# Kernel optimization log

Hardware: AMD Instinct MI355X
Metric: run time of the kernel (lower is better)

## Reference

```python
import jax, jax.numpy as jnp
import numpy as np
import math

PS = 8          # patch_size
OUT_C = 16      # out_channels
D_MODEL = 64
P_STATE = 32
BANDLIMIT = 1.0
STEP_SCALE = 1.0  # dt1 reference rate


def _ln(x, g, b, eps=1e-5):
    mu = jnp.mean(x, -1, keepdims=True)
    var = jnp.mean((x - mu) ** 2, -1, keepdims=True)
    return (x - mu) * jax.lax.rsqrt(var + eps) * g + b


def _forward(x, W_embed, b_embed, g1, beta1, Lambda_re, Lambda_im, B_re, B_im,
             C_re, C_im, D, log_step, g2, beta2, W_enc, W_dec, g3, beta3, W_out, b_out):
    b, t, h, w = x.shape
    hp, wp = h // PS, w // PS
    n = hp * wp
    # patchify: [b,t,h,w] -> [b,t,n,ps*ps]
    xp = x.reshape(b, t, hp, PS, wp, PS).transpose(0, 1, 2, 4, 3, 5).reshape(b, t, n, PS * PS)
    xe = xp @ W_embed.T + b_embed                              # [b,t,n,d]
    u = xe.transpose(0, 2, 1, 3).reshape(b * n, t, D_MODEL)    # [(b n), t, d]

    # ---- S5Block: pre-norm -> diagonal SSM -> gelu + residual -> GEGLU FFN ----
    fx = _ln(u, g1, beta1)
    Lam = Lambda_re + 1j * Lambda_im                           # [P] complex eigenvalues
    step = STEP_SCALE * jnp.exp(log_step)                      # [P]
    Lbar = jnp.exp(Lam * step)                                 # ZOH: A_bar
    Bbar = ((Lbar - 1.0) / Lam)[:, None] * (B_re + 1j * B_im)  # ZOH: B_bar [P,d]
    # bandlimit mask on C (freqs = step*|Im(Lambda)|/(2pi) < bandlimit/2)
    freqs = step * jnp.abs(Lambda_im) / (2.0 * math.pi)
    mask = (freqs < BANDLIMIT * 0.5).astype(C_re.dtype)
    Cc = (C_re + 1j * C_im) * mask[None, :]                    # [d,P]

    Bu = jnp.einsum('ntd,pd->ntp', fx.astype(jnp.complex64), Bbar)   # [(bn),t,P]
    A = jnp.broadcast_to(Lbar.astype(jnp.complex64), (1, t, P_STATE))

    def comb(e1, e2):
        a1, b1 = e1
        a2, b2 = e2
        return a1 * a2, a2 * b1 + b2

    _, xs = jax.lax.associative_scan(comb, (A, Bu), axis=1)    # x_k = A*x_{k-1} + Bu_k (x_0 = 0)
    ys = jnp.einsum('ntp,dp->ntd', xs, Cc).real + fx * D       # y = Re(C x) + D u
    xb = jax.nn.gelu(ys, approximate=False) + fx

    fx2 = _ln(xb, g2, beta2)
    enc = fx2 @ W_enc.T                                        # [(bn),t,2d]
    a, gate = jnp.split(enc, 2, axis=-1)
    xb = (a * jax.nn.gelu(gate, approximate=False)) @ W_dec.T + fx2

    # ---- take last timestep, project, unpatchify ----
    x_last = xb[:, -1, :]                                      # [(bn), d]
    proj = _ln(x_last, g3, beta3) @ W_out.T + b_out            # [(bn), C*ps*ps]
    y = proj.reshape(b, hp, wp, OUT_C, PS, PS).transpose(0, 3, 1, 4, 2, 5).reshape(b, OUT_C, h, w)
    return y


def setup_inputs() -> dict:
    key = jax.random.key(0)
    ks = jax.random.split(key, 12)
    d, P, pp = D_MODEL, P_STATE, PS * PS
    return dict(
        x=jax.random.normal(ks[0], (8, 15, 480, 640), jnp.float32),
        W_embed=jax.random.normal(ks[1], (d, pp), jnp.float32) / math.sqrt(pp),
        b_embed=jnp.zeros((d,), jnp.float32),
        g1=jnp.ones((d,), jnp.float32), beta1=jnp.zeros((d,), jnp.float32),
        Lambda_re=-0.5 * jnp.ones((P,), jnp.float32),
        Lambda_im=math.pi * (1.0 + jnp.arange(P, dtype=jnp.float32)),
        B_re=jax.random.normal(ks[2], (P, d), jnp.float32) / math.sqrt(d),
        B_im=jax.random.normal(ks[3], (P, d), jnp.float32) / math.sqrt(d),
        C_re=jax.random.normal(ks[4], (d, P), jnp.float32) / math.sqrt(P),
        C_im=jax.random.normal(ks[5], (d, P), jnp.float32) / math.sqrt(P),
        D=jax.random.normal(ks[6], (d,), jnp.float32),
        log_step=jax.random.uniform(ks[7], (P,), jnp.float32, math.log(1e-3), math.log(1e-1)),
        g2=jnp.ones((d,), jnp.float32), beta2=jnp.zeros((d,), jnp.float32),
        W_enc=jax.random.normal(ks[8], (2 * d, d), jnp.float32) / math.sqrt(d),
        W_dec=jax.random.normal(ks[9], (d, d), jnp.float32) / math.sqrt(d),
        g3=jnp.ones((d,), jnp.float32), beta3=jnp.zeros((d,), jnp.float32),
        W_out=jax.random.normal(ks[10], (OUT_C * pp, d), jnp.float32) / math.sqrt(d),
        b_out=jnp.zeros((OUT_C * pp,), jnp.float32),
    )


def reference(x, W_embed, b_embed, g1, beta1, Lambda_re, Lambda_im, B_re, B_im,
              C_re, C_im, D, log_step, g2, beta2, W_enc, W_dec, g3, beta3, W_out, b_out):
    return _forward(x, W_embed, b_embed, g1, beta1, Lambda_re, Lambda_im, B_re, B_im,
                    C_re, C_im, D, log_step, g2, beta2, W_enc, W_dec, g3, beta3, W_out, b_out)
```

## Files before the change

### kernel.cpp

```cpp
#include <hip/hip_runtime.h>
#include <math.h>


typedef __attribute__((ext_vector_type(8))) short short8;
typedef __attribute__((ext_vector_type(4))) float f32x4;

#define MFMA16(a, b, c) __builtin_amdgcn_mfma_f32_16x16x32_bf16((a), (b), (c), 0, 0, 0)

__device__ __forceinline__ short f2bf(float f) {
  union { float f; unsigned u; } v; v.f = f;
  unsigned r = (v.u + 0x7fffu + ((v.u >> 16) & 1u)) >> 16;
  return (short)r;
}
__device__ __forceinline__ float geluf(float x) {
  return 0.5f * x * (1.0f + erff(x * 0.70710678118654752f));
}
__device__ __forceinline__ short8 packfrag(const f32x4& a, const f32x4& b) {
  short8 o;
  o[0] = f2bf(a[0]); o[1] = f2bf(a[1]); o[2] = f2bf(a[2]); o[3] = f2bf(a[3]);
  o[4] = f2bf(b[0]); o[5] = f2bf(b[1]); o[6] = f2bf(b[2]); o[7] = f2bf(b[3]);
  return o;
}
__device__ __forceinline__ int ecmap(int i, int m) {
  return (i >> 1) * 32 + (m >> 2) * 8 + (i & 1) * 4 + (m & 3);
}
__device__ __forceinline__ int swz(int b) {
  return b ^ (((b >> 2) ^ (b >> 6)) & 0x60) ^ (((b >> 3) ^ (b >> 9)) & 0x10);
}
__device__ __forceinline__ void bbar_factors(const float* Lre, const float* Lim,
                                             const float* lstep, int p,
                                             float& fre, float& fim) {
  float st = expf(lstep[p]);
  float lr = Lre[p], li = Lim[p];
  float er = expf(lr * st);
  float lbr = er * cosf(li * st), lbi = er * sinf(li * st);
  float u = lbr - 1.0f, v = lbi;
  float den = lr * lr + li * li;
  fre = (u * lr + v * li) / den;
  fim = (v * lr - u * li) / den;
}

__global__ __launch_bounds__(256) void k0_prep(
    const float* __restrict__ W_embed, const float* __restrict__ g1,
    const float* __restrict__ be1, const float* __restrict__ Lre,
    const float* __restrict__ Lim, const float* __restrict__ Bre,
    const float* __restrict__ Bim, const float* __restrict__ Cre,
    const float* __restrict__ Cim, const float* __restrict__ lstep,
    const float* __restrict__ W_enc, const float* __restrict__ W_dec,
    const float* __restrict__ W_out, short* __restrict__ wimg,
    float* __restrict__ bu0) {
  const int bid = blockIdx.x;
  if (bid == 44) {
    int q = threadIdx.x;
    if (q < 64) {
      int c = q >> 5, p = q & 31;
      float fre, fim; bbar_factors(Lre, Lim, lstep, p, fre, fim);
      float s = 0.f;
      for (int d = 0; d < 64; ++d) {
        float br = Bre[p * 64 + d], bi = Bim[p * 64 + d];
        float val = c ? (fre * bi + fim * br) : (fre * br - fim * bi);
        s += be1[d] * val;
      }
      bu0[q] = s;
    }
    return;
  }
  const int w = threadIdx.x >> 6, lane = threadIdx.x & 63;
  const int m = lane & 15, qd = lane >> 4;
  const int f = bid * 4 + w;
  short v[8];
  if (f < 8) {
    int i = f >> 1, kt = f & 1, chan = ecmap(i, m), k0 = kt * 32 + qd * 8;
#pragma unroll
    for (int j = 0; j < 8; ++j) v[j] = f2bf(W_embed[chan * 64 + k0 + j]);
  } else if (f < 16) {
    int fi = f - 8, i = fi >> 1, kt = fi & 1;
    int comp = i & 1, p = (i >> 1) * 16 + m, d0 = kt * 32 + qd * 8;
    float fre, fim; bbar_factors(Lre, Lim, lstep, p, fre, fim);
#pragma unroll
    for (int j = 0; j < 8; ++j) {
      int d = d0 + j;
      float br = Bre[p * 64 + d], bi = Bim[p * 64 + d];
      float val = comp ? (fre * bi + fim * br) : (fre * br - fim * bi);
      v[j] = f2bf(g1[d] * val);
    }
  } else if (f < 24) {
    int fi = f - 16, i = fi >> 1, kt = fi & 1, chan = ecmap(i, m);
#pragma unroll
    for (int j = 0; j < 8; ++j) {
      int comp = j >> 2, p = kt * 16 + qd * 4 + (j & 3);
      float stp = expf(lstep[p]);
      float fr = stp * fabsf(Lim[p]) * (1.0f / 6.28318530717958648f);
      float msk = (fr < 0.5f) ? 1.f : 0.f;
      float val = comp ? -Cim[chan * 32 + p] * msk : Cre[chan * 32 + p] * msk;
      v[j] = f2bf(val);
    }
  } else if (f < 40) {
    int fi = f - 24, i = fi >> 1, kt = fi & 1;
    int row = (i < 4) ? ecmap(i, m) : 64 + ecmap(i - 4, m);
#pragma unroll
    for (int j = 0; j < 8; ++j) v[j] = f2bf(W_enc[row * 64 + kt * 32 + qd * 8 + j]);
  } else if (f < 48) {
    int fi = f - 40, i = fi >> 1, kt = fi & 1, row = ecmap(i, m);
#pragma unroll
    for (int j = 0; j < 8; ++j) v[j] = f2bf(W_dec[row * 64 + kt * 32 + qd * 8 + j]);
  } else {
    int fi = f - 48, i = fi >> 1, kt = fi & 1, row = i * 16 + m;
#pragma unroll
    for (int j = 0; j < 8; ++j) v[j] = f2bf(W_out[row * 64 + kt * 32 + qd * 8 + j]);
  }
  short8 sv;
#pragma unroll
  for (int j = 0; j < 8; ++j) sv[j] = v[j];
  *(short8*)&wimg[(f * 64 + lane) * 8] = sv;
}

__global__ __launch_bounds__(256) void k1_fused(
    const float* __restrict__ x, const short* __restrict__ wimg_g,
    const float* __restrict__ bu0_g, const float* __restrict__ Lre,
    const float* __restrict__ Lim, const float* __restrict__ lstep,
    const float* __restrict__ g1, const float* __restrict__ be1,
    const float* __restrict__ bemb, const float* __restrict__ Dv,
    const float* __restrict__ g2, const float* __restrict__ be2,
    const float* __restrict__ g3, const float* __restrict__ be3,
    const float* __restrict__ b_out, float* __restrict__ y) {
  __shared__ __align__(16) char smem[49152];
#define WF(id) (*(const short8*)(smem + (id) * 1024 + lane * 16))

  const int tid = threadIdx.x;
  const int wv = tid >> 6, lane = tid & 63;
  const int s = lane & 15, qd = lane >> 4;

  float4 wreg[4];
  {
    const float4* src = (const float4*)wimg_g;
#pragma unroll
    for (int j = 0; j < 4; ++j) wreg[j] = src[j * 256 + tid];
  }

  int cb[4];
  f32x4 bec[4], bu0c[4];
#pragma unroll
  for (int nt = 0; nt < 4; ++nt) {
    cb[nt] = (nt >> 1) * 32 + qd * 8 + (nt & 1) * 4;
    bec[nt] = *(const f32x4*)(bemb + cb[nt]);
    bu0c[nt] = *(const f32x4*)(bu0_g + (nt & 1) * 32 + (nt >> 1) * 16 + qd * 4);
  }
  f32x4 lbr[2], lbi[2];
#pragma unroll
  for (int k = 0; k < 2; ++k)
#pragma unroll
    for (int r = 0; r < 4; ++r) {
      int p = k * 16 + qd * 4 + r;
      float st = expf(lstep[p]);
      float er = expf(Lre[p] * st);
      lbr[k][r] = er * cosf(Lim[p] * st);
      lbi[k][r] = er * sinf(Lim[p] * st);
    }

  int off[4];
#pragma unroll
  for (int j = 0; j < 4; ++j) {
    int L = (wv * 4 + j) * 1024 + lane * 16;
    int b = swz(L);
    int c = b >> 4;
    int r = c >> 7, p = (c >> 1) & 63, h = c & 1;
    int seq = blockIdx.x * 64 + p;
    int b_i = seq / 4800, pr = seq % 4800;
    int ph = pr / 80, pw = pr % 80;
    off[j] = ((b_i * 15) * 480 + ph * 8 + r) * 640 + pw * 8 + h * 4;
  }
  int rb[4];
#pragma unroll
  for (int kt = 0; kt < 2; ++kt)
#pragma unroll
    for (int h = 0; h < 2; ++h) {
      int b = (kt * 4 + qd) * 2048 + (wv * 16 + s) * 32 + h * 16;
      rb[kt * 2 + h] = swz(b);
    }

#define STAGE(bufofs, tt)                                                     \
  {                                                                           \
    const float* gsrc = x + (tt) * 307200;                                    \
    char* lb = smem + (bufofs) + wv * 4096;                                   \
    _Pragma("unroll") for (int j = 0; j < 4; ++j)                             \
        __builtin_amdgcn_global_load_lds(                                     \
            (const __attribute__((address_space(1))) void*)(gsrc + off[j]),   \
            (__attribute__((address_space(3))) void*)(lb + j * 1024),         \
            16, 0, 0);                                                        \
  }

  const int sbase = (blockIdx.x * 4 + wv) * 16;

  STAGE(16384, 0);
  STAGE(32768, 1);
  {
    float4* wdst = (float4*)smem;
#pragma unroll
    for (int j = 0; j < 4; ++j) wdst[j * 256 + tid] = wreg[j];
  }
  asm volatile("s_waitcnt vmcnt(0) lgkmcnt(0)" ::: "memory");
  __builtin_amdgcn_s_barrier();

  const f32x4 zf = {0.f, 0.f, 0.f, 0.f};
  f32x4 state[4] = {zf, zf, zf, zf};
  f32x4 xh[4];

  for (int t = 0; t < 15; ++t) {
    const char* bufr = smem + 16384 + ((t & 1) << 14);
    f32x4 vcur[4];
#pragma unroll
    for (int q = 0; q < 4; ++q) vcur[q] = *(const f32x4*)(bufr + rb[q]);
    asm volatile("s_waitcnt lgkmcnt(0)" ::: "memory");
    __builtin_amdgcn_s_barrier();
    if (t < 13) STAGE(16384 + ((t & 1) << 14), t + 2);

    short8 pa0 = packfrag(vcur[0], vcur[1]);
    short8 pa1 = packfrag(vcur[2], vcur[3]);
    f32x4 c1[4];
#pragma unroll
    for (int i = 0; i < 4; ++i) {
      f32x4 acc = MFMA16(WF(i * 2), pa0, zf);
      acc = MFMA16(WF(i * 2 + 1), pa1, acc);
      c1[i] = acc + bec[i];
    }
    float sm = 0.f, sq = 0.f;
#pragma unroll
    for (int nt = 0; nt < 4; ++nt)
#pragma unroll
      for (int i = 0; i < 4; ++i) { sm += c1[nt][i]; sq += c1[nt][i] * c1[nt][i]; }
    sm += __shfl_xor(sm, 16); sq += __shfl_xor(sq, 16);
    sm += __shfl_xor(sm, 32); sq += __shfl_xor(sq, 32);
    float mean = sm * 0.015625f;
    float rstd = rsqrtf(sq * 0.015625f - mean * mean + 1e-5f);
#pragma unroll
    for (int nt = 0; nt < 4; ++nt) xh[nt] = (c1[nt] - mean) * rstd;
    short8 xa0 = packfrag(xh[0], xh[1]);
    short8 xa1 = packfrag(xh[2], xh[3]);
#pragma unroll
    for (int k = 0; k < 2; ++k) {
      f32x4 re = state[2 * k], im = state[2 * k + 1];
      state[2 * k]     = lbr[k] * re - lbi[k] * im + bu0c[2 * k];
      state[2 * k + 1] = lbr[k] * im + lbi[k] * re + bu0c[2 * k + 1];
    }
#pragma unroll
    for (int i = 0; i < 4; ++i) {
      state[i] = MFMA16(WF(8 + i * 2), xa0, state[i]);
      state[i] = MFMA16(WF(8 + i * 2 + 1), xa1, state[i]);
    }

    if (t < 14) {
      if (t < 13) asm volatile("s_waitcnt vmcnt(4)" ::: "memory");
      else        asm volatile("s_waitcnt vmcnt(0)" ::: "memory");
      __builtin_amdgcn_s_barrier();
    }
  }
#undef STAGE

  __syncthreads();
  {
    float4 hf[8];
    const float4* src = (const float4*)(wimg_g + 16 * 512);
#pragma unroll
    for (int j = 0; j < 8; ++j) hf[j] = src[j * 256 + tid];
    float4* dst = (float4*)(smem + 16384);
#pragma unroll
    for (int j = 0; j < 8; ++j) dst[j * 256 + tid] = hf[j];
  }
  __syncthreads();

  f32x4 g1c[4], b1c[4], Dc[4], g2c[4], b2c[4];
#pragma unroll
  for (int nt = 0; nt < 4; ++nt) {
    g1c[nt] = *(const f32x4*)(g1 + cb[nt]);
    b1c[nt] = *(const f32x4*)(be1 + cb[nt]);
    Dc[nt] = *(const f32x4*)(Dv + cb[nt]);
    g2c[nt] = *(const f32x4*)(g2 + cb[nt]);
    b2c[nt] = *(const f32x4*)(be2 + cb[nt]);
  }
  f32x4 fxl[4];
#pragma unroll
  for (int nt = 0; nt < 4; ++nt) fxl[nt] = xh[nt] * g1c[nt] + b1c[nt];

  short8 xsa0 = packfrag(state[0], state[1]);
  short8 xsa1 = packfrag(state[2], state[3]);
  f32x4 xbv[4];
#pragma unroll
  for (int i = 0; i < 4; ++i) {
    f32x4 acc = fxl[i] * Dc[i];
    acc = MFMA16(WF(16 + i * 2), xsa0, acc);
    acc = MFMA16(WF(16 + i * 2 + 1), xsa1, acc);
#pragma unroll
    for (int r = 0; r < 4; ++r) xbv[i][r] = geluf(acc[r]) + fxl[i][r];
  }
  float sm2 = 0.f, sq2 = 0.f;
#pragma unroll
  for (int nt = 0; nt < 4; ++nt)
#pragma unroll
    for (int i = 0; i < 4; ++i) { sm2 += xbv[nt][i]; sq2 += xbv[nt][i] * xbv[nt][i]; }
  sm2 += __shfl_xor(sm2, 16); sq2 += __shfl_xor(sq2, 16);
  sm2 += __shfl_xor(sm2, 32); sq2 += __shfl_xor(sq2, 32);
  float mean2 = sm2 * 0.015625f;
  float rstd2 = rsqrtf(sq2 * 0.015625f - mean2 * mean2 + 1e-5f);
  f32x4 fx2[4];
#pragma unroll
  for (int nt = 0; nt < 4; ++nt)
    fx2[nt] = (xbv[nt] - mean2) * rstd2 * g2c[nt] + b2c[nt];

  short8 fa0 = packfrag(fx2[0], fx2[1]);
  short8 fa1 = packfrag(fx2[2], fx2[3]);
  f32x4 e[8];
#pragma unroll
  for (int i = 0; i < 8; ++i) {
    f32x4 acc = MFMA16(WF(24 + i * 2), fa0, zf);
    e[i] = MFMA16(WF(24 + i * 2 + 1), fa1, acc);
  }
  f32x4 hv[4];
#pragma unroll
  for (int nt = 0; nt < 4; ++nt)
#pragma unroll
    for (int i = 0; i < 4; ++i) hv[nt][i] = e[nt][i] * geluf(e[nt + 4][i]);

  short8 ha0 = packfrag(hv[0], hv[1]);
  short8 ha1 = packfrag(hv[2], hv[3]);
  f32x4 xo[4];
#pragma unroll
  for (int i = 0; i < 4; ++i) {
    f32x4 acc = fx2[i];
    acc = MFMA16(WF(40 + i * 2), ha0, acc);
    xo[i] = MFMA16(WF(40 + i * 2 + 1), ha1, acc);
  }

  float sm3 = 0.f, sq3 = 0.f;
#pragma unroll
  for (int nt = 0; nt < 4; ++nt)
#pragma unroll
    for (int i = 0; i < 4; ++i) { sm3 += xo[nt][i]; sq3 += xo[nt][i] * xo[nt][i]; }
  sm3 += __shfl_xor(sm3, 16); sq3 += __shfl_xor(sq3, 16);
  sm3 += __shfl_xor(sm3, 32); sq3 += __shfl_xor(sq3, 32);
  float mean3 = sm3 * 0.015625f;
  float rstd3 = rsqrtf(sq3 * 0.015625f - mean3 * mean3 + 1e-5f);
  f32x4 z[4];
#pragma unroll
  for (int nt = 0; nt < 4; ++nt) {
    f32x4 g3c = *(const f32x4*)(g3 + cb[nt]);
    f32x4 b3c = *(const f32x4*)(be3 + cb[nt]);
    z[nt] = (xo[nt] - mean3) * rstd3 * g3c + b3c;
  }
  short8 za = packfrag(z[0], z[1]);
  short8 zb = packfrag(z[2], z[3]);

  const int seq = sbase + s;
  const int bi2 = seq / 4800, prr = seq % 4800;
  const int phh = prr / 80, pww = prr % 80;
  const int obase = (bi2 * 16 * 480 + phh * 8) * 640 + pww * 8;
  const short* wob = wimg_g + 48 * 512;

#pragma unroll 4
  for (int ntg = 0; ntg < 64; ++ntg) {
    short8 a0 = *(const short8*)&wob[(ntg * 2 + 0) * 512 + lane * 8];
    short8 a1 = *(const short8*)&wob[(ntg * 2 + 1) * 512 + lane * 8];
    int o0 = ntg * 16 + qd * 4;
    f32x4 acc = *(const f32x4*)(b_out + o0);
    acc = MFMA16(a0, za, acc);
    acc = MFMA16(a1, zb, acc);
    int c = o0 >> 6, pi = (o0 >> 3) & 7, pj = o0 & 7;
    *(f32x4*)&y[obase + c * 307200 + pi * 640 + pj] = acc;
  }
#undef WF
}

extern "C" void kernel_launch(void* const* d_in, const int* in_sizes, int n_in,
                              void* d_out, int out_size, void* d_ws, size_t ws_size,
                              hipStream_t stream) {
  const float* x       = (const float*)d_in[0];
  const float* W_embed = (const float*)d_in[1];
  const float* b_embed = (const float*)d_in[2];
  const float* g1      = (const float*)d_in[3];
  const float* beta1   = (const float*)d_in[4];
  const float* Lre     = (const float*)d_in[5];
  const float* Lim     = (const float*)d_in[6];
  const float* Bre     = (const float*)d_in[7];
  const float* Bim     = (const float*)d_in[8];
  const float* Cre     = (const float*)d_in[9];
  const float* Cim     = (const float*)d_in[10];
  const float* Dv      = (const float*)d_in[11];
  const float* lstep   = (const float*)d_in[12];
  const float* g2      = (const float*)d_in[13];
  const float* beta2   = (const float*)d_in[14];
  const float* W_enc   = (const float*)d_in[15];
  const float* W_dec   = (const float*)d_in[16];
  const float* g3      = (const float*)d_in[17];
  const float* beta3   = (const float*)d_in[18];
  const float* W_out   = (const float*)d_in[19];
  const float* b_out   = (const float*)d_in[20];
  float* y = (float*)d_out;

  short* wimg = (short*)d_ws;
  float* bu0 = (float*)((char*)d_ws + 176 * 1024);

  k0_prep<<<dim3(45), dim3(256), 0, stream>>>(W_embed, g1, beta1, Lre, Lim,
                                              Bre, Bim, Cre, Cim, lstep,
                                              W_enc, W_dec, W_out, wimg, bu0);
  k1_fused<<<dim3(600), dim3(256), 0, stream>>>(x, wimg, bu0, Lre, Lim, lstep,
                                                g1, beta1, b_embed, Dv, g2,
                                                beta2, g3, beta3, b_out, y);
}
```

Measured before the change: 327.8 us.

## Give each wave a private double-buffered staging region and drop per-step barriers

```diff
diff --git a/kernel.cpp b/kernel.cpp
--- a/kernel.cpp
+++ b/kernel.cpp
@@ -23,9 +23,6 @@
 }
 __device__ __forceinline__ int ecmap(int i, int m) {
   return (i >> 1) * 32 + (m >> 2) * 8 + (i & 1) * 4 + (m & 3);
-}
-__device__ __forceinline__ int swz(int b) {
-  return b ^ (((b >> 2) ^ (b >> 6)) & 0x60) ^ (((b >> 3) ^ (b >> 9)) & 0x10);
 }
 __device__ __forceinline__ void bbar_factors(const float* Lre, const float* Lim,
                                              const float* lstep, int p,
@@ -158,62 +155,58 @@
       lbi[k][r] = er * sinf(Lim[p] * st);
     }
 
-  int off[4];
+  const int sbase = (blockIdx.x * 4 + wv) * 16;
+  const int b_i = sbase / 4800;
+  const int prw = sbase % 4800;
+  const int phw = prw / 80, pw0 = prw % 80;
+  int offw[4];
 #pragma unroll
   for (int j = 0; j < 4; ++j) {
-    int L = (wv * 4 + j) * 1024 + lane * 16;
-    int b = swz(L);
-    int c = b >> 4;
-    int r = c >> 7, p = (c >> 1) & 63, h = c & 1;
-    int seq = blockIdx.x * 64 + p;
-    int b_i = seq / 4800, pr = seq % 4800;
-    int ph = pr / 80, pw = pr % 80;
-    off[j] = ((b_i * 15) * 480 + ph * 8 + r) * 640 + pw * 8 + h * 4;
+    int r = j * 2 + (lane >> 5);
+    offw[j] = ((b_i * 15) * 480 + phw * 8 + r) * 640 + pw0 * 8 + (lane & 31) * 4;
   }
   int rb[4];
 #pragma unroll
   for (int kt = 0; kt < 2; ++kt)
 #pragma unroll
-    for (int h = 0; h < 2; ++h) {
-      int b = (kt * 4 + qd) * 2048 + (wv * 16 + s) * 32 + h * 16;
-      rb[kt * 2 + h] = swz(b);
-    }
-
-#define STAGE(bufofs, tt)                                                     \
+    for (int h = 0; h < 2; ++h)
+      rb[kt * 2 + h] = (kt * 4 + qd) * 512 + s * 32 + h * 16;
+
+  char* const wbuf = smem + 16384 + wv * 8192;
+
+#define STAGEW(tsel, tt)                                                      \
   {                                                                           \
     const float* gsrc = x + (tt) * 307200;                                    \
-    char* lb = smem + (bufofs) + wv * 4096;                                   \
+    char* lb = wbuf + (tsel) * 4096;                                          \
     _Pragma("unroll") for (int j = 0; j < 4; ++j)                             \
         __builtin_amdgcn_global_load_lds(                                     \
-            (const __attribute__((address_space(1))) void*)(gsrc + off[j]),   \
+            (const __attribute__((address_space(1))) void*)(gsrc + offw[j]),  \
             (__attribute__((address_space(3))) void*)(lb + j * 1024),         \
             16, 0, 0);                                                        \
   }
 
-  const int sbase = (blockIdx.x * 4 + wv) * 16;
-
-  STAGE(16384, 0);
-  STAGE(32768, 1);
   {
     float4* wdst = (float4*)smem;
 #pragma unroll
     for (int j = 0; j < 4; ++j) wdst[j * 256 + tid] = wreg[j];
   }
-  asm volatile("s_waitcnt vmcnt(0) lgkmcnt(0)" ::: "memory");
-  __builtin_amdgcn_s_barrier();
+  __syncthreads();
+  STAGEW(0, 0);
+  STAGEW(1, 1);
 
   const f32x4 zf = {0.f, 0.f, 0.f, 0.f};
   f32x4 state[4] = {zf, zf, zf, zf};
   f32x4 xh[4];
 
   for (int t = 0; t < 15; ++t) {
-    const char* bufr = smem + 16384 + ((t & 1) << 14);
+    if (t < 14) asm volatile("s_waitcnt vmcnt(4)" ::: "memory");
+    else        asm volatile("s_waitcnt vmcnt(0)" ::: "memory");
+    const char* bufr = wbuf + ((t & 1) << 12);
     f32x4 vcur[4];
 #pragma unroll
     for (int q = 0; q < 4; ++q) vcur[q] = *(const f32x4*)(bufr + rb[q]);
     asm volatile("s_waitcnt lgkmcnt(0)" ::: "memory");
-    __builtin_amdgcn_s_barrier();
-    if (t < 13) STAGE(16384 + ((t & 1) << 14), t + 2);
+    if (t < 13) STAGEW(t & 1, t + 2);
 
     short8 pa0 = packfrag(vcur[0], vcur[1]);
     short8 pa1 = packfrag(vcur[2], vcur[3]);
@@ -248,14 +241,8 @@
       state[i] = MFMA16(WF(8 + i * 2), xa0, state[i]);
       state[i] = MFMA16(WF(8 + i * 2 + 1), xa1, state[i]);
     }
-
-    if (t < 14) {
-      if (t < 13) asm volatile("s_waitcnt vmcnt(4)" ::: "memory");
-      else        asm volatile("s_waitcnt vmcnt(0)" ::: "memory");
-      __builtin_amdgcn_s_barrier();
-    }
-  }
-#undef STAGE
+  }
+#undef STAGEW
 
   __syncthreads();
   {
```

New measurement: 325.5 us. About the same (-0.7%).

## Map each block to one patch-row band with five waves and contiguous loads

Applied to the files above, without the earlier changes.

```diff
diff --git a/kernel.cpp b/kernel.cpp
--- a/kernel.cpp
+++ b/kernel.cpp
@@ -23,9 +23,6 @@
 }
 __device__ __forceinline__ int ecmap(int i, int m) {
   return (i >> 1) * 32 + (m >> 2) * 8 + (i & 1) * 4 + (m & 3);
-}
-__device__ __forceinline__ int swz(int b) {
-  return b ^ (((b >> 2) ^ (b >> 6)) & 0x60) ^ (((b >> 3) ^ (b >> 9)) & 0x10);
 }
 __device__ __forceinline__ void bbar_factors(const float* Lre, const float* Lim,
                                              const float* lstep, int p,
@@ -115,7 +112,7 @@
   *(short8*)&wimg[(f * 64 + lane) * 8] = sv;
 }
 
-__global__ __launch_bounds__(256) void k1_fused(
+__global__ __launch_bounds__(320) void k1_fused(
     const float* __restrict__ x, const short* __restrict__ wimg_g,
     const float* __restrict__ bu0_g, const float* __restrict__ Lre,
     const float* __restrict__ Lim, const float* __restrict__ lstep,
@@ -124,19 +121,12 @@
     const float* __restrict__ g2, const float* __restrict__ be2,
     const float* __restrict__ g3, const float* __restrict__ be3,
     const float* __restrict__ b_out, float* __restrict__ y) {
-  __shared__ __align__(16) char smem[49152];
+  __shared__ __align__(16) char smem[57344];
 #define WF(id) (*(const short8*)(smem + (id) * 1024 + lane * 16))
 
   const int tid = threadIdx.x;
   const int wv = tid >> 6, lane = tid & 63;
   const int s = lane & 15, qd = lane >> 4;
-
-  float4 wreg[4];
-  {
-    const float4* src = (const float4*)wimg_g;
-#pragma unroll
-    for (int j = 0; j < 4; ++j) wreg[j] = src[j * 256 + tid];
-  }
 
   int cb[4];
   f32x4 bec[4], bu0c[4];
@@ -158,46 +148,35 @@
       lbi[k][r] = er * sinf(Lim[p] * st);
     }
 
-  int off[4];
-#pragma unroll
-  for (int j = 0; j < 4; ++j) {
-    int L = (wv * 4 + j) * 1024 + lane * 16;
-    int b = swz(L);
-    int c = b >> 4;
-    int r = c >> 7, p = (c >> 1) & 63, h = c & 1;
-    int seq = blockIdx.x * 64 + p;
-    int b_i = seq / 4800, pr = seq % 4800;
-    int ph = pr / 80, pw = pr % 80;
-    off[j] = ((b_i * 15) * 480 + ph * 8 + r) * 640 + pw * 8 + h * 4;
-  }
+  const int b_i = blockIdx.x / 60;
+  const int ph = blockIdx.x % 60;
+  const int tb0 = ((b_i * 15) * 480 + ph * 8) * 640;
+  const int sbase = blockIdx.x * 80 + wv * 16;
   int rb[4];
 #pragma unroll
   for (int kt = 0; kt < 2; ++kt)
 #pragma unroll
-    for (int h = 0; h < 2; ++h) {
-      int b = (kt * 4 + qd) * 2048 + (wv * 16 + s) * 32 + h * 16;
-      rb[kt * 2 + h] = swz(b);
-    }
+    for (int h = 0; h < 2; ++h)
+      rb[kt * 2 + h] = (kt * 4 + qd) * 2560 + (wv * 16 + s) * 32 + h * 16;
 
 #define STAGE(bufofs, tt)                                                     \
   {                                                                           \
-    const float* gsrc = x + (tt) * 307200;                                    \
+    const float* gsrc = x + tb0 + (tt) * 307200 + wv * 1024;                  \
     char* lb = smem + (bufofs) + wv * 4096;                                   \
     _Pragma("unroll") for (int j = 0; j < 4; ++j)                             \
         __builtin_amdgcn_global_load_lds(                                     \
-            (const __attribute__((address_space(1))) void*)(gsrc + off[j]),   \
+            (const __attribute__((address_space(1))) void*)(gsrc + j * 256 +  \
+                                                            lane * 4),        \
             (__attribute__((address_space(3))) void*)(lb + j * 1024),         \
             16, 0, 0);                                                        \
   }
 
-  const int sbase = (blockIdx.x * 4 + wv) * 16;
-
   STAGE(16384, 0);
-  STAGE(32768, 1);
+  STAGE(36864, 1);
   {
     float4* wdst = (float4*)smem;
-#pragma unroll
-    for (int j = 0; j < 4; ++j) wdst[j * 256 + tid] = wreg[j];
+    const float4* wsrc = (const float4*)wimg_g;
+    for (int i = tid; i < 1024; i += 320) wdst[i] = wsrc[i];
   }
   asm volatile("s_waitcnt vmcnt(0) lgkmcnt(0)" ::: "memory");
   __builtin_amdgcn_s_barrier();
@@ -207,13 +186,13 @@
   f32x4 xh[4];
 
   for (int t = 0; t < 15; ++t) {
-    const char* bufr = smem + 16384 + ((t & 1) << 14);
+    const char* bufr = smem + 16384 + (t & 1) * 20480;
     f32x4 vcur[4];
 #pragma unroll
     for (int q = 0; q < 4; ++q) vcur[q] = *(const f32x4*)(bufr + rb[q]);
     asm volatile("s_waitcnt lgkmcnt(0)" ::: "memory");
     __builtin_amdgcn_s_barrier();
-    if (t < 13) STAGE(16384 + ((t & 1) << 14), t + 2);
+    if (t < 13) STAGE(16384 + (t & 1) * 20480, t + 2);
 
     short8 pa0 = packfrag(vcur[0], vcur[1]);
     short8 pa1 = packfrag(vcur[2], vcur[3]);
@@ -259,13 +238,9 @@
 
   __syncthreads();
   {
-    float4 hf[8];
+    float4* dst = (float4*)(smem + 16384);
     const float4* src = (const float4*)(wimg_g + 16 * 512);
-#pragma unroll
-    for (int j = 0; j < 8; ++j) hf[j] = src[j * 256 + tid];
-    float4* dst = (float4*)(smem + 16384);
-#pragma unroll
-    for (int j = 0; j < 8; ++j) dst[j * 256 + tid] = hf[j];
+    for (int i = tid; i < 2048; i += 320) dst[i] = src[i];
   }
   __syncthreads();
 
@@ -402,7 +377,7 @@
   k0_prep<<<dim3(45), dim3(256), 0, stream>>>(W_embed, g1, beta1, Lre, Lim,
                                               Bre, Bim, Cre, Cim, lstep,
                                               W_enc, W_dec, W_out, wimg, bu0);
-  k1_fused<<<dim3(600), dim3(256), 0, stream>>>(x, wimg, bu0, Lre, Lim, lstep,
+  k1_fused<<<dim3(480), dim3(320), 0, stream>>>(x, wimg, bu0, Lre, Lim, lstep,
                                                 g1, beta1, b_embed, Dv, g2,
                                                 beta2, g3, beta3, b_out, y);
 }
```

Result: slower. 338.6 us (+3.3%).
